# Kernel optimization log

Hardware: AMD Instinct MI355X
Metric: run time of the kernel (lower is better)

## Reference

```python
import jax, jax.numpy as jnp
import numpy as np
from math import sqrt


def setup_inputs() -> dict:
    key0 = jax.random.key(0)
    ks = jax.random.split(key0, 7)
    N, H, E, D, S = 32, 16, 128, 128, 2047
    return {
        "query": jax.random.normal(ks[0], (N, H, E), dtype=jnp.float32),
        "key": jax.random.normal(ks[1], (N, H, E), dtype=jnp.float32),
        "value": jax.random.normal(ks[2], (N, H, D), dtype=jnp.float32),
        "keys_cache": jax.random.normal(ks[3], (N, H, S, E), dtype=jnp.float32),
        "values_cache": jax.random.normal(ks[4], (N, H, S, D), dtype=jnp.float32),
        "w_pre": jax.random.normal(ks[5], (H, H), dtype=jnp.float32) * (1.0 / sqrt(H)),
        "w_post": jax.random.normal(ks[6], (H, H), dtype=jnp.float32) * (1.0 / sqrt(H)),
    }


def reference(query, key, value, keys_cache, values_cache, w_pre, w_post):
    # Single recurrent decode step with talking-heads mixing (dropout in eval mode).
    N, H, E = query.shape
    softmax_temp = 1.0 / sqrt(E)
    # Append current key/value to the cache: [N,H,S+1,E] / [N,H,S+1,D]
    keys = jnp.concatenate([keys_cache, key[:, :, None, :]], axis=2)
    values = jnp.concatenate([values_cache, value[:, :, None, :]], axis=2)
    # Scores: [N,H,S]
    QK = jnp.einsum('nhe,nhse->nhs', query, keys)
    # Pre-softmax talking heads (1x1 conv over head axis): out_g = sum_h w[g,h] * in_h
    QK = jnp.einsum('gh,nhs->ngs', w_pre, QK)
    A = jax.nn.softmax(softmax_temp * QK, axis=-1)
    # Post-softmax talking heads
    A = jnp.einsum('gh,nhs->ngs', w_post, A)
    # Weighted value readout: [N,H,D]
    V = jnp.einsum('nhs,nhsd->nhd', A, values)
    return V, keys, values
```

## Files before the change

kernel.cpp:

```cpp
#include <hip/hip_runtime.h>
#include <cstddef>

constexpr int N_  = 32;
constexpr int H_  = 16;
constexpr int E_  = 128;
constexpr int D_  = 128;
constexpr int S_  = 2047;
constexpr int SP1 = 2048;
constexpr int NH  = N_ * H_;

constexpr int ROWS_PER_BLOCK = 256;
constexpr int CHUNKS = SP1 / ROWS_PER_BLOCK;

__global__ __launch_bounds__(256) void k1_keys_scores(
    const float* __restrict__ query, const float* __restrict__ key,
    const float* __restrict__ keys_cache,
    float* __restrict__ keys_out, float* __restrict__ scores)
{
  const int bid   = blockIdx.x;
  const int nh    = bid / CHUNKS;
  const int chunk = bid % CHUNKS;
  const int tid   = threadIdx.x;
  const int wave  = tid >> 6;
  const int lane  = tid & 63;
  const int half  = lane >> 5;
  const int lcol  = lane & 31;

  const float4 q4 = *reinterpret_cast<const float4*>(query + (size_t)nh * E_ + lcol * 4);

  #pragma unroll 4
  for (int it = 0; it < ROWS_PER_BLOCK / 8; ++it) {
    const int r = it * 8 + wave * 2 + half;
    const int s = chunk * ROWS_PER_BLOCK + r;
    const float* src = (s < S_) ? (keys_cache + ((size_t)nh * S_ + s) * E_)
                                : (key + (size_t)nh * E_);
    float4 k4 = *reinterpret_cast<const float4*>(src + lcol * 4);
    *reinterpret_cast<float4*>(keys_out + ((size_t)nh * SP1 + s) * E_ + lcol * 4) = k4;

    float p = q4.x * k4.x + q4.y * k4.y + q4.z * k4.z + q4.w * k4.w;
    p += __shfl_xor(p, 1);
    p += __shfl_xor(p, 2);
    p += __shfl_xor(p, 4);
    p += __shfl_xor(p, 8);
    p += __shfl_xor(p, 16);
    if (lcol == 0) scores[(size_t)nh * SP1 + s] = p;
  }
}

__global__ __launch_bounds__(256) void k2_mix(
    const float* __restrict__ w, const float* __restrict__ in,
    float* __restrict__ out)
{
  __shared__ float wl[H_ * H_];
  const int tid = threadIdx.x;
  if (tid < H_ * H_) wl[tid] = w[tid];
  __syncthreads();

  const int g = blockIdx.x * 256 + tid;
  const int n = g / SP1;
  const int s = g % SP1;

  float v[H_];
  #pragma unroll
  for (int h = 0; h < H_; ++h)
    v[h] = in[((size_t)(n * H_ + h)) * SP1 + s];

  #pragma unroll
  for (int gh = 0; gh < H_; ++gh) {
    float acc = 0.0f;
    #pragma unroll
    for (int h = 0; h < H_; ++h) acc += wl[gh * H_ + h] * v[h];
    out[((size_t)(n * H_ + gh)) * SP1 + s] = acc;
  }
}

__global__ __launch_bounds__(256) void k2_softmax(float* __restrict__ a)
{
  __shared__ float vals[SP1];
  __shared__ float red[8];
  const int row = blockIdx.x;
  const int tid = threadIdx.x;
  const int wave = tid >> 6;
  const int lane = tid & 63;
  const float temp = 0.08838834764831845f;

  float* rp = a + (size_t)row * SP1;

  float lmax = -3.4e38f;
  #pragma unroll
  for (int k = 0; k < SP1 / 256; ++k) {
    float x = rp[tid + k * 256] * temp;
    vals[tid + k * 256] = x;
    lmax = fmaxf(lmax, x);
  }
  #pragma unroll
  for (int m = 1; m <= 32; m <<= 1) lmax = fmaxf(lmax, __shfl_xor(lmax, m));
  if (lane == 0) red[wave] = lmax;
  __syncthreads();
  const float bmax = fmaxf(fmaxf(red[0], red[1]), fmaxf(red[2], red[3]));

  float lsum = 0.0f;
  #pragma unroll
  for (int k = 0; k < SP1 / 256; ++k) {
    float e = __expf(vals[tid + k * 256] - bmax);
    vals[tid + k * 256] = e;
    lsum += e;
  }
  #pragma unroll
  for (int m = 1; m <= 32; m <<= 1) lsum += __shfl_xor(lsum, m);
  if (lane == 0) red[4 + wave] = lsum;
  __syncthreads();
  const float inv = 1.0f / (red[4] + red[5] + red[6] + red[7]);

  #pragma unroll
  for (int k = 0; k < SP1 / 256; ++k)
    rp[tid + k * 256] = vals[tid + k * 256] * inv;
}

__global__ __launch_bounds__(256) void k3_values(
    const float* __restrict__ value, const float* __restrict__ values_cache,
    const float* __restrict__ a2, float* __restrict__ values_out,
    float* __restrict__ partials)
{
  __shared__ float lds[8][128];
  const int bid   = blockIdx.x;
  const int nh    = bid / CHUNKS;
  const int chunk = bid % CHUNKS;
  const int tid   = threadIdx.x;
  const int wave  = tid >> 6;
  const int lane  = tid & 63;
  const int half  = lane >> 5;
  const int lcol  = lane & 31;
  const int group = wave * 2 + half;

  float4 acc = {0.0f, 0.0f, 0.0f, 0.0f};

  #pragma unroll 4
  for (int it = 0; it < ROWS_PER_BLOCK / 8; ++it) {
    const int r = it * 8 + wave * 2 + half;
    const int s = chunk * ROWS_PER_BLOCK + r;
    const float* src = (s < S_) ? (values_cache + ((size_t)nh * S_ + s) * D_)
                                : (value + (size_t)nh * D_);
    float4 v4 = *reinterpret_cast<const float4*>(src + lcol * 4);
    *reinterpret_cast<float4*>(values_out + ((size_t)nh * SP1 + s) * D_ + lcol * 4) = v4;

    const float w = a2[(size_t)nh * SP1 + s];
    acc.x += w * v4.x;
    acc.y += w * v4.y;
    acc.z += w * v4.z;
    acc.w += w * v4.w;
  }

  *reinterpret_cast<float4*>(&lds[group][lcol * 4]) = acc;
  __syncthreads();
  if (tid < 128) {
    float sum = 0.0f;
    #pragma unroll
    for (int gq = 0; gq < 8; ++gq) sum += lds[gq][tid];
    partials[(size_t)bid * 128 + tid] = sum;
  }
}

__global__ __launch_bounds__(256) void k4_reduce(
    const float* __restrict__ partials, float* __restrict__ v_out)
{
  const int g = blockIdx.x * 256 + threadIdx.x;
  const int nh = g >> 7;
  const int d = g & 127;
  float s = 0.0f;
  #pragma unroll
  for (int c = 0; c < CHUNKS; ++c)
    s += partials[((size_t)(nh * CHUNKS + c)) * 128 + d];
  v_out[g] = s;
}

extern "C" void kernel_launch(void* const* d_in, const int* in_sizes, int n_in,
                              void* d_out, int out_size, void* d_ws, size_t ws_size,
                              hipStream_t stream) {
  const float* query        = (const float*)d_in[0];
  const float* key          = (const float*)d_in[1];
  const float* value        = (const float*)d_in[2];
  const float* keys_cache   = (const float*)d_in[3];
  const float* values_cache = (const float*)d_in[4];
  const float* w_pre        = (const float*)d_in[5];
  const float* w_post       = (const float*)d_in[6];

  float* out = (float*)d_out;
  float* v_out      = out;
  float* keys_out   = out + (size_t)NH * D_;
  float* values_out = keys_out + (size_t)NH * SP1 * E_;

  float* buf0     = (float*)d_ws;
  float* buf1     = buf0 + (size_t)NH * SP1;
  float* partials = buf1 + (size_t)NH * SP1;

  k1_keys_scores<<<NH * CHUNKS, 256, 0, stream>>>(query, key, keys_cache,
                                                  keys_out, buf0);
  k2_mix<<<(N_ * SP1) / 256, 256, 0, stream>>>(w_pre, buf0, buf1);
  k2_softmax<<<NH, 256, 0, stream>>>(buf1);
  k2_mix<<<(N_ * SP1) / 256, 256, 0, stream>>>(w_post, buf1, buf0);
  k3_values<<<NH * CHUNKS, 256, 0, stream>>>(value, values_cache, buf0,
                                             values_out, partials);
  k4_reduce<<<(NH * 128) / 256, 256, 0, stream>>>(partials, v_out);
}
```

Measured before the change: 450.1 us.

## Fuse talking-heads mixes into softmax and value kernels, use nontemporal streaming

```diff
diff --git a/kernel.cpp b/kernel.cpp
--- a/kernel.cpp
+++ b/kernel.cpp
@@ -11,6 +11,8 @@
 
 constexpr int ROWS_PER_BLOCK = 256;
 constexpr int CHUNKS = SP1 / ROWS_PER_BLOCK;
+
+typedef float vfloat4 __attribute__((ext_vector_type(4)));
 
 __global__ __launch_bounds__(256) void k1_keys_scores(
     const float* __restrict__ query, const float* __restrict__ key,
@@ -26,16 +28,18 @@
   const int half  = lane >> 5;
   const int lcol  = lane & 31;
 
-  const float4 q4 = *reinterpret_cast<const float4*>(query + (size_t)nh * E_ + lcol * 4);
-
-  #pragma unroll 4
+  const vfloat4 q4 = *reinterpret_cast<const vfloat4*>(query + (size_t)nh * E_ + lcol * 4);
+
+  #pragma unroll 8
   for (int it = 0; it < ROWS_PER_BLOCK / 8; ++it) {
     const int r = it * 8 + wave * 2 + half;
     const int s = chunk * ROWS_PER_BLOCK + r;
     const float* src = (s < S_) ? (keys_cache + ((size_t)nh * S_ + s) * E_)
                                 : (key + (size_t)nh * E_);
-    float4 k4 = *reinterpret_cast<const float4*>(src + lcol * 4);
-    *reinterpret_cast<float4*>(keys_out + ((size_t)nh * SP1 + s) * E_ + lcol * 4) = k4;
+    vfloat4 k4 = __builtin_nontemporal_load(
+        reinterpret_cast<const vfloat4*>(src + lcol * 4));
+    __builtin_nontemporal_store(k4,
+        reinterpret_cast<vfloat4*>(keys_out + ((size_t)nh * SP1 + s) * E_ + lcol * 4));
 
     float p = q4.x * k4.x + q4.y * k4.y + q4.z * k4.z + q4.w * k4.w;
     p += __shfl_xor(p, 1);
@@ -47,51 +51,34 @@
   }
 }
 
-__global__ __launch_bounds__(256) void k2_mix(
-    const float* __restrict__ w, const float* __restrict__ in,
-    float* __restrict__ out)
-{
-  __shared__ float wl[H_ * H_];
-  const int tid = threadIdx.x;
-  if (tid < H_ * H_) wl[tid] = w[tid];
-  __syncthreads();
-
-  const int g = blockIdx.x * 256 + tid;
-  const int n = g / SP1;
-  const int s = g % SP1;
-
-  float v[H_];
-  #pragma unroll
-  for (int h = 0; h < H_; ++h)
-    v[h] = in[((size_t)(n * H_ + h)) * SP1 + s];
-
-  #pragma unroll
-  for (int gh = 0; gh < H_; ++gh) {
-    float acc = 0.0f;
-    #pragma unroll
-    for (int h = 0; h < H_; ++h) acc += wl[gh * H_ + h] * v[h];
-    out[((size_t)(n * H_ + gh)) * SP1 + s] = acc;
-  }
-}
-
-__global__ __launch_bounds__(256) void k2_softmax(float* __restrict__ a)
-{
-  __shared__ float vals[SP1];
+__global__ __launch_bounds__(256) void k2_mix_softmax(
+    const float* __restrict__ w_pre, const float* __restrict__ scores,
+    float* __restrict__ a_out)
+{
+  __shared__ float wl[H_];
   __shared__ float red[8];
-  const int row = blockIdx.x;
+  const int n = blockIdx.x >> 4;
+  const int g = blockIdx.x & 15;
   const int tid = threadIdx.x;
   const int wave = tid >> 6;
   const int lane = tid & 63;
   const float temp = 0.08838834764831845f;
 
-  float* rp = a + (size_t)row * SP1;
-
+  if (tid < H_) wl[tid] = w_pre[g * H_ + tid];
+  __syncthreads();
+
+  const float* base = scores + (size_t)n * H_ * SP1;
+  float x[SP1 / 256];
   float lmax = -3.4e38f;
   #pragma unroll
   for (int k = 0; k < SP1 / 256; ++k) {
-    float x = rp[tid + k * 256] * temp;
-    vals[tid + k * 256] = x;
-    lmax = fmaxf(lmax, x);
+    const int s = tid + k * 256;
+    float acc = 0.0f;
+    #pragma unroll
+    for (int h = 0; h < H_; ++h) acc += wl[h] * base[(size_t)h * SP1 + s];
+    acc *= temp;
+    x[k] = acc;
+    lmax = fmaxf(lmax, acc);
   }
   #pragma unroll
   for (int m = 1; m <= 32; m <<= 1) lmax = fmaxf(lmax, __shfl_xor(lmax, m));
@@ -102,8 +89,8 @@
   float lsum = 0.0f;
   #pragma unroll
   for (int k = 0; k < SP1 / 256; ++k) {
-    float e = __expf(vals[tid + k * 256] - bmax);
-    vals[tid + k * 256] = e;
+    float e = __expf(x[k] - bmax);
+    x[k] = e;
     lsum += e;
   }
   #pragma unroll
@@ -112,17 +99,19 @@
   __syncthreads();
   const float inv = 1.0f / (red[4] + red[5] + red[6] + red[7]);
 
+  float* out = a_out + (size_t)(n * H_ + g) * SP1;
   #pragma unroll
   for (int k = 0; k < SP1 / 256; ++k)
-    rp[tid + k * 256] = vals[tid + k * 256] * inv;
+    out[tid + k * 256] = x[k] * inv;
 }
 
 __global__ __launch_bounds__(256) void k3_values(
     const float* __restrict__ value, const float* __restrict__ values_cache,
-    const float* __restrict__ a2, float* __restrict__ values_out,
-    float* __restrict__ partials)
+    const float* __restrict__ a, const float* __restrict__ w_post,
+    float* __restrict__ values_out, float* __restrict__ partials)
 {
   __shared__ float lds[8][128];
+  __shared__ float a2[ROWS_PER_BLOCK];
   const int bid   = blockIdx.x;
   const int nh    = bid / CHUNKS;
   const int chunk = bid % CHUNKS;
@@ -133,25 +122,43 @@
   const int lcol  = lane & 31;
   const int group = wave * 2 + half;
 
-  float4 acc = {0.0f, 0.0f, 0.0f, 0.0f};
-
-  #pragma unroll 4
+  {
+    const int n = nh >> 4;
+    const int g = nh & 15;
+    const int s = chunk * ROWS_PER_BLOCK + tid;
+    const float* abase = a + (size_t)n * H_ * SP1 + s;
+    const float* wrow  = w_post + g * H_;
+    float acc = 0.0f;
+    #pragma unroll
+    for (int h = 0; h < H_; ++h) acc += wrow[h] * abase[(size_t)h * SP1];
+    a2[tid] = acc;
+  }
+  __syncthreads();
+
+  float accx = 0.0f, accy = 0.0f, accz = 0.0f, accw = 0.0f;
+
+  #pragma unroll 8
   for (int it = 0; it < ROWS_PER_BLOCK / 8; ++it) {
     const int r = it * 8 + wave * 2 + half;
     const int s = chunk * ROWS_PER_BLOCK + r;
     const float* src = (s < S_) ? (values_cache + ((size_t)nh * S_ + s) * D_)
                                 : (value + (size_t)nh * D_);
-    float4 v4 = *reinterpret_cast<const float4*>(src + lcol * 4);
-    *reinterpret_cast<float4*>(values_out + ((size_t)nh * SP1 + s) * D_ + lcol * 4) = v4;
-
-    const float w = a2[(size_t)nh * SP1 + s];
-    acc.x += w * v4.x;
-    acc.y += w * v4.y;
-    acc.z += w * v4.z;
-    acc.w += w * v4.w;
-  }
-
-  *reinterpret_cast<float4*>(&lds[group][lcol * 4]) = acc;
+    vfloat4 v4 = __builtin_nontemporal_load(
+        reinterpret_cast<const vfloat4*>(src + lcol * 4));
+    __builtin_nontemporal_store(v4,
+        reinterpret_cast<vfloat4*>(values_out + ((size_t)nh * SP1 + s) * D_ + lcol * 4));
+
+    const float w = a2[r];
+    accx += w * v4.x;
+    accy += w * v4.y;
+    accz += w * v4.z;
+    accw += w * v4.w;
+  }
+
+  lds[group][lcol * 4 + 0] = accx;
+  lds[group][lcol * 4 + 1] = accy;
+  lds[group][lcol * 4 + 2] = accz;
+  lds[group][lcol * 4 + 3] = accw;
   __syncthreads();
   if (tid < 128) {
     float sum = 0.0f;
@@ -196,10 +203,8 @@
 
   k1_keys_scores<<<NH * CHUNKS, 256, 0, stream>>>(query, key, keys_cache,
                                                   keys_out, buf0);
-  k2_mix<<<(N_ * SP1) / 256, 256, 0, stream>>>(w_pre, buf0, buf1);
-  k2_softmax<<<NH, 256, 0, stream>>>(buf1);
-  k2_mix<<<(N_ * SP1) / 256, 256, 0, stream>>>(w_post, buf1, buf0);
-  k3_values<<<NH * CHUNKS, 256, 0, stream>>>(value, values_cache, buf0,
+  k2_mix_softmax<<<NH, 256, 0, stream>>>(w_pre, buf0, buf1);
+  k3_values<<<NH * CHUNKS, 256, 0, stream>>>(value, values_cache, buf1, w_post,
                                              values_out, partials);
   k4_reduce<<<(NH * 128) / 256, 256, 0, stream>>>(partials, v_out);
 }
```

Result: no change. 442.2 us (-1.8%).
